# Performance work log

Hardware: AMD Instinct MI355X
Metric: run time of the kernel (lower is better)

The kernel has to match this reference:

```python
import jax, jax.numpy as jnp
import numpy as np

B, S, D = 4, 2048, 1024
E, H = 1024, 16
HD = E // H
TEMPERATURE = 1.0


def setup_inputs() -> dict:
    key = jax.random.key(0)
    ks = jax.random.split(key, 6)
    x = jax.random.normal(ks[0], (B, S, D), dtype=jnp.float32)
    src_key_padding_mask = jnp.zeros((B, S), dtype=bool)  # unused by module
    matrix_mask = jax.random.normal(ks[1], (B, S, S), dtype=jnp.float32)
    # Xavier-uniform linear weights (torch Linear stores [out, in])
    lim_qkv = float(np.sqrt(6.0 / (D + 3 * E)))
    qkv_w = jax.random.uniform(ks[2], (3 * E, D), dtype=jnp.float32, minval=-lim_qkv, maxval=lim_qkv)
    qkv_b = jnp.zeros((3 * E,), dtype=jnp.float32)
    lim_o = float(np.sqrt(6.0 / (E + E)))
    o_w = jax.random.uniform(ks[3], (E, E), dtype=jnp.float32, minval=-lim_o, maxval=lim_o)
    o_b = jnp.zeros((E,), dtype=jnp.float32)
    return {"x": x, "src_key_padding_mask": src_key_padding_mask, "matrix_mask": matrix_mask,
            "qkv_w": qkv_w, "qkv_b": qkv_b, "o_w": o_w, "o_b": o_b}


def reference(x, src_key_padding_mask, matrix_mask, qkv_w, qkv_b, o_w, o_b):
    b, s, _ = x.shape
    qkv = x @ qkv_w.T + qkv_b                      # [B,S,3E]
    qkv = qkv.reshape(b, s, H, 3 * HD).transpose(0, 2, 1, 3)  # [B,H,S,3*HD]
    q, k, v = jnp.split(qkv, 3, axis=-1)           # each [B,H,S,HD]
    scale = 1.0 / np.sqrt(HD)
    logits = jnp.einsum('bhqd,bhkd->bhqk', q, k) * scale + matrix_mask[:, None, :, :]
    attn = jax.nn.softmax(logits / TEMPERATURE, axis=-1)  # [B,H,S,S]
    # dropout=0.0, eval mode -> no-op
    values = jnp.einsum('bhqk,bhkd->bhqd', attn, v)       # [B,H,S,HD]
    values = values.transpose(0, 2, 1, 3).reshape(b, s, E)
    o = values @ o_w.T + o_b                       # [B,S,E]
    attention_mean = jnp.mean(attn, axis=1)        # [B,S,S]
    return (o, attention_mean)
```

## Files before the change

kernel.cpp:

```cpp
#include <hip/hip_runtime.h>

#define B_ 4
#define S_ 2048
#define D_ 1024
#define E_ 1024
#define H_ 16
#define HD_ 64
#define SCALE 0.125f
#define LOG2E 1.44269504f
#define C1_ (SCALE * LOG2E)

typedef __bf16 bf16;
typedef __bf16 bf16x8 __attribute__((ext_vector_type(8)));
typedef __bf16 bf16x4 __attribute__((ext_vector_type(4)));
typedef float f32x4 __attribute__((ext_vector_type(4)));
typedef _Float16 f16x8 __attribute__((ext_vector_type(8)));
typedef _Float16 f16x4 __attribute__((ext_vector_type(4)));

static __device__ __forceinline__ f32x4 mfma16(bf16x8 a, bf16x8 b, f32x4 c) {
  return __builtin_amdgcn_mfma_f32_16x16x32_bf16(a, b, c, 0, 0, 0);
}

typedef __attribute__((address_space(3))) void lvoid;
typedef const __attribute__((address_space(1))) void gvoid;
static __device__ __forceinline__ void gload16(const void* g, void* l) {
  __builtin_amdgcn_global_load_lds((gvoid*)g, (lvoid*)l, 16, 0, 0);
}

static __device__ __forceinline__ float exp2a(float x) {
  float r;
  asm("v_exp_f32 %0, %1" : "=v"(r) : "v"(x));
  return r;
}

static __device__ __forceinline__ int rsw(int row) {
  return (row & 3) | (((row >> 3) & 1) << 2);
}

__global__ void k_cvt(const float* __restrict__ in, bf16* __restrict__ out, int n4) {
  int i = blockIdx.x * 256 + threadIdx.x;
  if (i >= n4) return;
  float4 v = reinterpret_cast<const float4*>(in)[i];
  bf16x4 o = { (bf16)v.x, (bf16)v.y, (bf16)v.z, (bf16)v.w };
  reinterpret_cast<bf16x4*>(out)[i] = o;
}

__global__ void k_cvt16(const float* __restrict__ in, _Float16* __restrict__ out, int n4) {
  int i = blockIdx.x * 256 + threadIdx.x;
  if (i >= n4) return;
  float4 v = reinterpret_cast<const float4*>(in)[i];
  f16x4 o = { (_Float16)(v.x * LOG2E), (_Float16)(v.y * LOG2E),
              (_Float16)(v.z * LOG2E), (_Float16)(v.w * LOG2E) };
  reinterpret_cast<f16x4*>(out)[i] = o;
}

__global__ __launch_bounds__(256) void k_qkv(const bf16* __restrict__ xb,
                                             const bf16* __restrict__ wb,
                                             const float* __restrict__ qkvb,
                                             bf16* __restrict__ Qw,
                                             bf16* __restrict__ Kw,
                                             bf16* __restrict__ Vtw) {
  __shared__ __align__(16) bf16 lA[128 * 32];
  __shared__ __align__(16) bf16 lB[128 * 32];
  const int tid = threadIdx.x, lane = tid & 63, wv = tid >> 6;
  const int u = lane >> 4, c = lane & 15;
  const int wr = wv >> 1, wc = wv & 1;
  const int m0 = blockIdx.y * 128;
  const int n0 = blockIdx.x * 128;
  const int sr = tid >> 2, sk = (tid & 3) * 8;
  const bf16* gA = xb + (size_t)(m0 + sr) * D_ + sk;
  const bf16* gB = wb + (size_t)(n0 + sr) * D_ + sk;
  bf16* lpA = lA + wv * 512;
  bf16* lpB = lB + wv * 512;
  f32x4 acc[4][4] = {};
  for (int k0 = 0; k0 < D_; k0 += 32) {
    gload16(gA + k0, lpA);
    gload16(gA + 64 * D_ + k0, lpA + 2048);
    gload16(gB + k0, lpB);
    gload16(gB + 64 * D_ + k0, lpB + 2048);
    __syncthreads();
    bf16x8 af[4], bfr[4];
#pragma unroll
    for (int m = 0; m < 4; ++m)
      af[m] = *(const bf16x8*)(lA + (wr * 64 + m * 16 + c) * 32 + u * 8);
#pragma unroll
    for (int n = 0; n < 4; ++n)
      bfr[n] = *(const bf16x8*)(lB + (wc * 64 + n * 16 + c) * 32 + u * 8);
#pragma unroll
    for (int m = 0; m < 4; ++m)
#pragma unroll
      for (int n = 0; n < 4; ++n)
        acc[m][n] = mfma16(af[m], bfr[n], acc[m][n]);
    __syncthreads();
  }
#pragma unroll
  for (int n = 0; n < 4; ++n) {
    int nn = n0 + wc * 64 + n * 16 + c;
    float bias = qkvb[nn];
    int h = nn / 192;
    int rem = nn - h * 192;
#pragma unroll
    for (int m = 0; m < 4; ++m) {
#pragma unroll
      for (int r = 0; r < 4; ++r) {
        int q = m0 + wr * 64 + m * 16 + 4 * u + r;
        int bb = q >> 11, s = q & 2047;
        bf16 v = (bf16)(acc[m][n][r] + bias);
        if (rem < 64)       Qw[((bb * H_ + h) * S_ + s) * HD_ + rem] = v;
        else if (rem < 128) Kw[((bb * H_ + h) * S_ + s) * HD_ + (rem - 64)] = v;
        else                Vtw[((bb * H_ + h) * HD_ + (rem - 128)) * S_ + s] = v;
      }
    }
  }
}

#define PV_TILE2(HC, HN, BS, KT, PF)                                          \
  {                                                                           \
    f32x4 sA[4], sB[4];                                                       \
    _Pragma("unroll")                                                         \
    for (int f = 0; f < 4; ++f) {                                             \
      int rk = 32 * (f & 1) + 8 * (c >> 2) + 4 * (f >> 1) + (c & 3);          \
      int sw = rsw(rk);                                                       \
      bf16x8 k0 = *(const bf16x8*)&kl[BS][rk * 64 + ((u ^ sw) * 8)];          \
      bf16x8 k1 = *(const bf16x8*)&kl[BS][rk * 64 + (((4 + u) ^ sw) * 8)];    \
      f32x4 a = {};                                                           \
      a = mfma16(k0, aqA0, a);                                                \
      a = mfma16(k1, aqA1, a);                                                \
      sA[f] = a;                                                              \
      f32x4 bb2 = {};                                                         \
      bb2 = mfma16(k0, aqB0, bb2);                                            \
      bb2 = mfma16(k1, aqB1, bb2);                                            \
      sB[f] = bb2;                                                            \
    }                                                                         \
    if (PF) {                                                                 \
      const bf16* ksrc = Kb + (size_t)((KT) + 1) * 64 * HD_;                  \
      gload16(ksrc + ksw1, (bf16*)kl[(BS) ^ 1] + wv * 512);                   \
      gload16(ksrc + ksw2, (bf16*)kl[(BS) ^ 1] + 2048 + wv * 512);            \
      const bf16* vsrc = Vb + (size_t)((KT) + 1) * 64;                        \
      gload16(vsrc + vsw1, (bf16*)vl[(BS) ^ 1] + wv * 512);                   \
      gload16(vsrc + vsw2, (bf16*)vl[(BS) ^ 1] + 2048 + wv * 512);            \
      const _Float16* nA = bmrA + ((KT) + 1) * 64 + 8 * u;                    \
      const _Float16* nB = bmrB + ((KT) + 1) * 64 + 8 * u;                    \
      HN[0] = *(const f16x8*)(nA);                                            \
      HN[1] = *(const f16x8*)(nA + 32);                                       \
      HN[2] = *(const f16x8*)(nB);                                            \
      HN[3] = *(const f16x8*)(nB + 32);                                       \
    }                                                                         \
    float pA[16], pB[16];                                                     \
    _Pragma("unroll")                                                         \
    for (int f = 0; f < 4; ++f) {                                             \
      _Pragma("unroll")                                                       \
      for (int j = 0; j < 4; ++j) {                                           \
        float p = exp2a(sA[f][j] * C1_ + (float)HC[f & 1][4 * (f >> 1) + j]); \
        lsumA += p;                                                           \
        pA[f * 4 + j] = p;                                                    \
        float q2 = exp2a(sB[f][j] * C1_ +                                     \
                         (float)HC[2 + (f & 1)][4 * (f >> 1) + j]);           \
        lsumB += q2;                                                          \
        pB[f * 4 + j] = q2;                                                   \
      }                                                                       \
    }                                                                         \
    bf16x8 bpA0 = { (bf16)pA[0],  (bf16)pA[1],  (bf16)pA[2],  (bf16)pA[3],    \
                    (bf16)pA[8],  (bf16)pA[9],  (bf16)pA[10], (bf16)pA[11] }; \
    bf16x8 bpA1 = { (bf16)pA[4],  (bf16)pA[5],  (bf16)pA[6],  (bf16)pA[7],    \
                    (bf16)pA[12], (bf16)pA[13], (bf16)pA[14], (bf16)pA[15] }; \
    bf16x8 bpB0 = { (bf16)pB[0],  (bf16)pB[1],  (bf16)pB[2],  (bf16)pB[3],    \
                    (bf16)pB[8],  (bf16)pB[9],  (bf16)pB[10], (bf16)pB[11] }; \
    bf16x8 bpB1 = { (bf16)pB[4],  (bf16)pB[5],  (bf16)pB[6],  (bf16)pB[7],    \
                    (bf16)pB[12], (bf16)pB[13], (bf16)pB[14], (bf16)pB[15] }; \
    __builtin_amdgcn_s_setprio(1);                                            \
    _Pragma("unroll")                                                         \
    for (int g = 0; g < 4; ++g) {                                             \
      int rv = g * 16 + c;                                                    \
      int swv = rsw(rv);                                                      \
      bf16x8 v0 = *(const bf16x8*)&vl[BS][rv * 64 + ((u ^ swv) * 8)];         \
      bf16x8 v1 = *(const bf16x8*)&vl[BS][rv * 64 + (((4 + u) ^ swv) * 8)];   \
      accA[g] = mfma16(v0, bpA0, accA[g]);                                    \
      accA[g] = mfma16(v1, bpA1, accA[g]);                                    \
      accB[g] = mfma16(v0, bpB0, accB[g]);                                    \
      accB[g] = mfma16(v1, bpB1, accB[g]);                                    \
    }                                                                         \
    __builtin_amdgcn_s_setprio(0);                                            \
    __syncthreads();                                                          \
  }

__global__ __launch_bounds__(256) void k_pv(const bf16* __restrict__ Qw,
                                            const bf16* __restrict__ Kw,
                                            const bf16* __restrict__ Vtw,
                                            const _Float16* __restrict__ bmask,
                                            float* __restrict__ li_ws,
                                            bf16* __restrict__ valw) {
  __shared__ __align__(16) bf16 kl[2][64 * 64];
  __shared__ __align__(16) bf16 vl[2][64 * 64];
  const int tid = threadIdx.x, lane = tid & 63, wv = tid >> 6;
  const int u = lane >> 4, c = lane & 15;
  const int qt = blockIdx.x, h = blockIdx.y, b = blockIdx.z;
  const bf16* Qb = Qw + (size_t)(b * H_ + h) * S_ * HD_;
  const bf16* Kb = Kw + (size_t)(b * H_ + h) * S_ * HD_;
  const bf16* Vb = Vtw + (size_t)(b * H_ + h) * HD_ * S_;
  const int qrA = qt * 128 + wv * 32 + c;
  const int qrB = qrA + 16;
  bf16x8 aqA0 = *(const bf16x8*)(Qb + (size_t)qrA * HD_ + u * 8);
  bf16x8 aqA1 = *(const bf16x8*)(Qb + (size_t)qrA * HD_ + 32 + u * 8);
  bf16x8 aqB0 = *(const bf16x8*)(Qb + (size_t)qrB * HD_ + u * 8);
  bf16x8 aqB1 = *(const bf16x8*)(Qb + (size_t)qrB * HD_ + 32 + u * 8);
  const _Float16* bmrA = bmask + (size_t)b * S_ * S_ + (size_t)qrA * S_;
  const _Float16* bmrB = bmask + (size_t)b * S_ * S_ + (size_t)qrB * S_;
  const int r1 = tid >> 3, s1 = (tid & 7) ^ rsw(tid >> 3);
  const int g2i = tid + 256;
  const int r2 = g2i >> 3, s2 = (g2i & 7) ^ rsw(g2i >> 3);
  const int ksw1 = (r1 * 8 + s1) * 8, ksw2 = (r2 * 8 + s2) * 8;
  const int vsw1 = r1 * S_ + s1 * 8, vsw2 = r2 * S_ + s2 * 8;
  gload16(Kb + ksw1, (bf16*)kl[0] + wv * 512);
  gload16(Kb + ksw2, (bf16*)kl[0] + 2048 + wv * 512);
  gload16(Vb + vsw1, (bf16*)vl[0] + wv * 512);
  gload16(Vb + vsw2, (bf16*)vl[0] + 2048 + wv * 512);
  f16x8 hmA[4], hmB[4];
  hmA[0] = *(const f16x8*)(bmrA + 8 * u);
  hmA[1] = *(const f16x8*)(bmrA + 32 + 8 * u);
  hmA[2] = *(const f16x8*)(bmrB + 8 * u);
  hmA[3] = *(const f16x8*)(bmrB + 32 + 8 * u);
  f32x4 accA[4] = {}, accB[4] = {};
  float lsumA = 0.f, lsumB = 0.f;
  __syncthreads();
  for (int kt2 = 0; kt2 < 16; ++kt2) {
    PV_TILE2(hmA, hmB, 0, 2 * kt2, true);
    PV_TILE2(hmB, hmA, 1, 2 * kt2 + 1, (kt2 < 15));
  }
  lsumA += __shfl_xor(lsumA, 16, 64);
  lsumA += __shfl_xor(lsumA, 32, 64);
  lsumB += __shfl_xor(lsumB, 16, 64);
  lsumB += __shfl_xor(lsumB, 32, 64);
  float liA = 1.f / lsumA, liB = 1.f / lsumB;
  if (u == 0) {
    li_ws[(b * H_ + h) * S_ + qrA] = liA;
    li_ws[(b * H_ + h) * S_ + qrB] = liB;
  }
#pragma unroll
  for (int g = 0; g < 4; ++g) {
    bf16x4 pkA = { (bf16)(accA[g][0] * liA), (bf16)(accA[g][1] * liA),
                   (bf16)(accA[g][2] * liA), (bf16)(accA[g][3] * liA) };
    *(bf16x4*)(&valw[(size_t)(b * S_ + qrA) * E_ + h * HD_ + g * 16 + 4 * u]) = pkA;
    bf16x4 pkB = { (bf16)(accB[g][0] * liB), (bf16)(accB[g][1] * liB),
                   (bf16)(accB[g][2] * liB), (bf16)(accB[g][3] * liB) };
    *(bf16x4*)(&valw[(size_t)(b * S_ + qrB) * E_ + h * HD_ + g * 16 + 4 * u]) = pkB;
  }
}

#define MEAN_PHASE(QC0, QC1, QN0, QN1, BS, HH, PF)                             \
  {                                                                            \
    bf16x8 kf[8];                                                              \
    _Pragma("unroll")                                                          \
    for (int f = 0; f < 4; ++f) {                                              \
      int row = f * 16 + c;                                                    \
      int sw = row & 7;                                                        \
      kf[2 * f]     = *(const bf16x8*)&kl2[BS][row * 64 + ((u ^ sw) * 8)];     \
      kf[2 * f + 1] = *(const bf16x8*)&kl2[BS][row * 64 + (((4 + u) ^ sw) * 8)];\
    }                                                                          \
    if (PF) {                                                                  \
      const bf16* ksrc = Kw + (size_t)(bh0 + (HH) + 1) * S_ * HD_ +            \
                         (size_t)kt * 64 * HD_;                                \
      gload16(ksrc + sw1, (bf16*)kl2[(BS) ^ 1] + wv * 512);                    \
      gload16(ksrc + sw2, (bf16*)kl2[(BS) ^ 1] + 2048 + wv * 512);             \
      const bf16* Qn = Qw + (size_t)(bh0 + (HH) + 1) * S_ * HD_ +              \
                       (size_t)(qrow0 + c) * HD_ + u * 8;                      \
      QN0 = *(const bf16x8*)(Qn);                                              \
      QN1 = *(const bf16x8*)(Qn + 32);                                         \
    }                                                                          \
    float ll = li_l[(HH) * 64 + wv * 16 + c];                                  \
    f32x4 accf[4];                                                             \
    _Pragma("unroll")                                                          \
    for (int f = 0; f < 4; ++f) {                                              \
      f32x4 a = {};                                                            \
      a = mfma16(kf[2 * f], QC0, a);                                           \
      a = mfma16(kf[2 * f + 1], QC1, a);                                       \
      accf[f] = a;                                                             \
    }                                                                          \
    _Pragma("unroll")                                                          \
    for (int f = 0; f < 4; ++f) {                                              \
      _Pragma("unroll")                                                        \
      for (int j = 0; j < 4; ++j)                                              \
        macc[f][j] += exp2a(accf[f][j] * C1_ + mreg[f][j]) * ll;               \
    }                                                                          \
    __syncthreads();                                                           \
  }

__global__ __launch_bounds__(256) void k_mean(const bf16* __restrict__ Qw,
                                              const bf16* __restrict__ Kw,
                                              const _Float16* __restrict__ bmask,
                                              const float* __restrict__ li_ws,
                                              float* __restrict__ mean_out) {
  __shared__ float li_l[H_ * 64];
  __shared__ __align__(16) bf16 kl2[2][64 * 64];
  const int tid = threadIdx.x, lane = tid & 63, wv = tid >> 6;
  const int u = lane >> 4, c = lane & 15;
  const int qt = blockIdx.x, kt = blockIdx.y, b = blockIdx.z;
  const int bh0 = b * H_;
  for (int i = tid; i < H_ * 64; i += 256) {
    int hh = i >> 6, q = i & 63;
    li_l[i] = li_ws[(bh0 + hh) * S_ + qt * 64 + q];
  }
  const int qrow0 = qt * 64 + wv * 16;
  f32x4 mreg[4];
  {
    const _Float16* bmp = bmask + (size_t)b * S_ * S_ +
                          (size_t)(qrow0 + c) * S_ + (size_t)kt * 64 + 4 * u;
#pragma unroll
    for (int f = 0; f < 4; ++f) {
      f16x4 hv = *(const f16x4*)(bmp + f * 16);
      f32x4 mv = { (float)hv[0], (float)hv[1], (float)hv[2], (float)hv[3] };
      mreg[f] = mv;
    }
  }
  const int gg1 = wv * 64 + lane;
  const int gg2 = gg1 + 256;
  const int sw1 = (gg1 ^ ((gg1 >> 3) & 7)) * 8;
  const int sw2 = (gg2 ^ ((gg2 >> 3) & 7)) * 8;
  {
    const bf16* K0 = Kw + (size_t)bh0 * S_ * HD_ + (size_t)kt * 64 * HD_;
    gload16(K0 + sw1, (bf16*)kl2[0] + wv * 512);
    gload16(K0 + sw2, (bf16*)kl2[0] + 2048 + wv * 512);
  }
  bf16x8 qA0, qA1, qB0, qB1;
  {
    const bf16* Q0 = Qw + (size_t)bh0 * S_ * HD_ + (size_t)(qrow0 + c) * HD_ + u * 8;
    qA0 = *(const bf16x8*)Q0;
    qA1 = *(const bf16x8*)(Q0 + 32);
  }
  f32x4 macc[4] = {};
  __syncthreads();
  for (int h2 = 0; h2 < 8; ++h2) {
    MEAN_PHASE(qA0, qA1, qB0, qB1, 0, 2 * h2, true);
    MEAN_PHASE(qB0, qB1, qA0, qA1, 1, 2 * h2 + 1, (h2 < 7));
  }
#pragma unroll
  for (int f = 0; f < 4; ++f) {
    f32x4 mo = macc[f] * (1.f / 16.f);
    *(f32x4*)&mean_out[(size_t)b * S_ * S_ + (size_t)(qrow0 + c) * S_ +
                       (size_t)kt * 64 + f * 16 + 4 * u] = mo;
  }
}

__global__ __launch_bounds__(256) void k_oproj(const bf16* __restrict__ vb,
                                               const bf16* __restrict__ wo,
                                               const float* __restrict__ ob,
                                               float* __restrict__ out) {
  __shared__ __align__(16) bf16 lA[128 * 32];
  __shared__ __align__(16) bf16 lB[128 * 32];
  const int tid = threadIdx.x, lane = tid & 63, wv = tid >> 6;
  const int u = lane >> 4, c = lane & 15;
  const int wr = wv >> 1, wc = wv & 1;
  const int m0 = blockIdx.y * 128;
  const int n0 = blockIdx.x * 128;
  const int sr = tid >> 2, sk = (tid & 3) * 8;
  const bf16* gA = vb + (size_t)(m0 + sr) * E_ + sk;
  const bf16* gB = wo + (size_t)(n0 + sr) * E_ + sk;
  bf16* lpA = lA + wv * 512;
  bf16* lpB = lB + wv * 512;
  f32x4 acc[4][4] = {};
  for (int k0 = 0; k0 < E_; k0 += 32) {
    gload16(gA + k0, lpA);
    gload16(gA + 64 * E_ + k0, lpA + 2048);
    gload16(gB + k0, lpB);
    gload16(gB + 64 * E_ + k0, lpB + 2048);
    __syncthreads();
    bf16x8 af[4], bfr[4];
#pragma unroll
    for (int m = 0; m < 4; ++m)
      af[m] = *(const bf16x8*)(lA + (wr * 64 + m * 16 + c) * 32 + u * 8);
#pragma unroll
    for (int n = 0; n < 4; ++n)
      bfr[n] = *(const bf16x8*)(lB + (wc * 64 + n * 16 + c) * 32 + u * 8);
#pragma unroll
    for (int m = 0; m < 4; ++m)
#pragma unroll
      for (int n = 0; n < 4; ++n)
        acc[m][n] = mfma16(af[m], bfr[n], acc[m][n]);
    __syncthreads();
  }
#pragma unroll
  for (int n = 0; n < 4; ++n) {
    int nn = n0 + wc * 64 + n * 16 + c;
    float bias = ob[nn];
#pragma unroll
    for (int m = 0; m < 4; ++m) {
#pragma unroll
      for (int r = 0; r < 4; ++r) {
        int q = m0 + wr * 64 + m * 16 + 4 * u + r;
        out[(size_t)q * E_ + nn] = acc[m][n][r] + bias;
      }
    }
  }
}

extern "C" void kernel_launch(void* const* d_in, const int* in_sizes, int n_in,
                              void* d_out, int out_size, void* d_ws, size_t ws_size,
                              hipStream_t stream) {
  const float* x    = (const float*)d_in[0];
  const float* mmsk = (const float*)d_in[2];
  const float* qkvw = (const float*)d_in[3];
  const float* qkvb = (const float*)d_in[4];
  const float* ow   = (const float*)d_in[5];
  const float* ob   = (const float*)d_in[6];

  char* ws = (char*)d_ws;
  bf16* xb  = (bf16*)(ws);
  bf16* wb  = (bf16*)(ws + (16u << 20));
  bf16* owb = (bf16*)(ws + (22u << 20));
  bf16* Qw  = (bf16*)(ws + (24u << 20));
  bf16* Kw  = (bf16*)(ws + (40u << 20));
  bf16* Vtw = (bf16*)(ws + (56u << 20));
  float* li_ws = (float*)(ws + (16u << 20));
  bf16* values = xb;

  float* out_o    = (float*)d_out;
  float* out_mean = out_o + (size_t)B_ * S_ * E_;
  _Float16* bmask = (_Float16*)out_o;

  k_cvt<<<dim3(2097152 / 256), 256, 0, stream>>>(x, xb, 2097152);
  k_cvt<<<dim3(786432 / 256), 256, 0, stream>>>(qkvw, wb, 786432);
  k_cvt<<<dim3(262144 / 256), 256, 0, stream>>>(ow, owb, 262144);
  k_cvt16<<<dim3(4194304 / 256), 256, 0, stream>>>(mmsk, bmask, 4194304);
  k_qkv<<<dim3(24, 64), 256, 0, stream>>>(xb, wb, qkvb, Qw, Kw, Vtw);
  k_pv<<<dim3(16, 16, 4), 256, 0, stream>>>(Qw, Kw, Vtw, bmask, li_ws, values);
  k_mean<<<dim3(32, 32, 4), 256, 0, stream>>>(Qw, Kw, bmask, li_ws, out_mean);
  k_oproj<<<dim3(8, 64), 256, 0, stream>>>(values, owb, ob, out_o);
}
```

Baseline: 344.3 us.

## Issue K/V prefetch before QK compute and double query rows per mean block

In the attention-PV and mean kernels, the async global-to-LDS prefetch of the next K/V tile is now issued at the start of each tile, before the QK MFMAs. The full __syncthreads is replaced by a partial vmcnt wait plus s_barrier so the prefetch can stay in flight across iterations. The mean kernel now handles 128 query rows per block (two 64-row halves), so each K tile loaded into LDS serves twice as much work, and the grid halves. The mask is kept as f16 in registers and the exp is fused into the MFMA loop. This raises register pressure and relies on hand-counted vmcnt values being correct.

```diff
diff --git a/kernel.cpp b/kernel.cpp
--- a/kernel.cpp
+++ b/kernel.cpp
@@ -116,6 +116,15 @@
 
 #define PV_TILE2(HC, HN, BS, KT, PF)                                          \
   {                                                                           \
+    if (PF) {                                                                 \
+      const bf16* ksrc = Kb + (size_t)((KT) + 1) * 64 * HD_;                  \
+      gload16(ksrc + ksw1, (bf16*)kl[(BS) ^ 1] + wv * 512);                   \
+      gload16(ksrc + ksw2, (bf16*)kl[(BS) ^ 1] + 2048 + wv * 512);            \
+      const bf16* vsrc = Vb + (size_t)((KT) + 1) * 64;                        \
+      gload16(vsrc + vsw1, (bf16*)vl[(BS) ^ 1] + wv * 512);                   \
+      gload16(vsrc + vsw2, (bf16*)vl[(BS) ^ 1] + 2048 + wv * 512);            \
+      __builtin_amdgcn_sched_barrier(0);                                      \
+    }                                                                         \
     f32x4 sA[4], sB[4];                                                       \
     _Pragma("unroll")                                                         \
     for (int f = 0; f < 4; ++f) {                                             \
@@ -133,12 +142,6 @@
       sB[f] = bb2;                                                            \
     }                                                                         \
     if (PF) {                                                                 \
-      const bf16* ksrc = Kb + (size_t)((KT) + 1) * 64 * HD_;                  \
-      gload16(ksrc + ksw1, (bf16*)kl[(BS) ^ 1] + wv * 512);                   \
-      gload16(ksrc + ksw2, (bf16*)kl[(BS) ^ 1] + 2048 + wv * 512);            \
-      const bf16* vsrc = Vb + (size_t)((KT) + 1) * 64;                        \
-      gload16(vsrc + vsw1, (bf16*)vl[(BS) ^ 1] + wv * 512);                   \
-      gload16(vsrc + vsw2, (bf16*)vl[(BS) ^ 1] + 2048 + wv * 512);            \
       const _Float16* nA = bmrA + ((KT) + 1) * 64 + 8 * u;                    \
       const _Float16* nB = bmrB + ((KT) + 1) * 64 + 8 * u;                    \
       HN[0] = *(const f16x8*)(nA);                                            \
@@ -181,7 +184,8 @@
       accB[g] = mfma16(v1, bpB1, accB[g]);                                    \
     }                                                                         \
     __builtin_amdgcn_s_setprio(0);                                            \
-    __syncthreads();                                                          \
+    asm volatile("s_waitcnt vmcnt(4) lgkmcnt(0)" ::: "memory");               \
+    __builtin_amdgcn_s_barrier();                                             \
   }
 
 __global__ __launch_bounds__(256) void k_pv(const bf16* __restrict__ Qw,
@@ -247,8 +251,15 @@
   }
 }
 
-#define MEAN_PHASE(QC0, QC1, QN0, QN1, BS, HH, PF)                             \
+#define MEAN_PHASE(QC0, QC1, QC2, QC3, QN0, QN1, QN2, QN3, BS, HH, PF)         \
   {                                                                            \
+    if (PF) {                                                                  \
+      const bf16* ksrc = Kw + (size_t)(bh0 + (HH) + 1) * S_ * HD_ +            \
+                         (size_t)kt * 64 * HD_;                                \
+      gload16(ksrc + sw1, (bf16*)kl2[(BS) ^ 1] + wv * 512);                    \
+      gload16(ksrc + sw2, (bf16*)kl2[(BS) ^ 1] + 2048 + wv * 512);             \
+      __builtin_amdgcn_sched_barrier(0);                                       \
+    }                                                                          \
     bf16x8 kf[8];                                                              \
     _Pragma("unroll")                                                          \
     for (int f = 0; f < 4; ++f) {                                              \
@@ -258,31 +269,31 @@
       kf[2 * f + 1] = *(const bf16x8*)&kl2[BS][row * 64 + (((4 + u) ^ sw) * 8)];\
     }                                                                          \
     if (PF) {                                                                  \
-      const bf16* ksrc = Kw + (size_t)(bh0 + (HH) + 1) * S_ * HD_ +            \
-                         (size_t)kt * 64 * HD_;                                \
-      gload16(ksrc + sw1, (bf16*)kl2[(BS) ^ 1] + wv * 512);                    \
-      gload16(ksrc + sw2, (bf16*)kl2[(BS) ^ 1] + 2048 + wv * 512);             \
       const bf16* Qn = Qw + (size_t)(bh0 + (HH) + 1) * S_ * HD_ +              \
                        (size_t)(qrow0 + c) * HD_ + u * 8;                      \
       QN0 = *(const bf16x8*)(Qn);                                              \
       QN1 = *(const bf16x8*)(Qn + 32);                                         \
+      QN2 = *(const bf16x8*)(Qn + 64 * HD_);                                   \
+      QN3 = *(const bf16x8*)(Qn + 64 * HD_ + 32);                              \
     }                                                                          \
-    float ll = li_l[(HH) * 64 + wv * 16 + c];                                  \
-    f32x4 accf[4];                                                             \
+    float llA = li_l[(HH) * 128 + wv * 16 + c];                                \
+    float llB = li_l[(HH) * 128 + 64 + wv * 16 + c];                           \
     _Pragma("unroll")                                                          \
     for (int f = 0; f < 4; ++f) {                                              \
       f32x4 a = {};                                                            \
       a = mfma16(kf[2 * f], QC0, a);                                           \
       a = mfma16(kf[2 * f + 1], QC1, a);                                       \
-      accf[f] = a;                                                             \
+      f32x4 bb = {};                                                           \
+      bb = mfma16(kf[2 * f], QC2, bb);                                         \
+      bb = mfma16(kf[2 * f + 1], QC3, bb);                                     \
+      _Pragma("unroll")                                                        \
+      for (int j = 0; j < 4; ++j) {                                            \
+        maccA[f][j] += exp2a(a[j] * C1_ + (float)mhA[f][j]) * llA;             \
+        maccB[f][j] += exp2a(bb[j] * C1_ + (float)mhB[f][j]) * llB;            \
+      }                                                                        \
     }                                                                          \
-    _Pragma("unroll")                                                          \
-    for (int f = 0; f < 4; ++f) {                                              \
-      _Pragma("unroll")                                                        \
-      for (int j = 0; j < 4; ++j)                                              \
-        macc[f][j] += exp2a(accf[f][j] * C1_ + mreg[f][j]) * ll;               \
-    }                                                                          \
-    __syncthreads();                                                           \
+    asm volatile("s_waitcnt vmcnt(4) lgkmcnt(0)" ::: "memory");                \
+    __builtin_amdgcn_s_barrier();                                              \
   }
 
 __global__ __launch_bounds__(256) void k_mean(const bf16* __restrict__ Qw,
@@ -290,26 +301,26 @@
                                               const _Float16* __restrict__ bmask,
                                               const float* __restrict__ li_ws,
                                               float* __restrict__ mean_out) {
-  __shared__ float li_l[H_ * 64];
+  __shared__ float li_l[H_ * 128];
   __shared__ __align__(16) bf16 kl2[2][64 * 64];
   const int tid = threadIdx.x, lane = tid & 63, wv = tid >> 6;
   const int u = lane >> 4, c = lane & 15;
   const int qt = blockIdx.x, kt = blockIdx.y, b = blockIdx.z;
   const int bh0 = b * H_;
-  for (int i = tid; i < H_ * 64; i += 256) {
-    int hh = i >> 6, q = i & 63;
-    li_l[i] = li_ws[(bh0 + hh) * S_ + qt * 64 + q];
-  }
-  const int qrow0 = qt * 64 + wv * 16;
-  f32x4 mreg[4];
+  for (int i = tid; i < H_ * 128; i += 256) {
+    int hh = i >> 7, q = i & 127;
+    li_l[i] = li_ws[(bh0 + hh) * S_ + qt * 128 + q];
+  }
+  const int qrow0 = qt * 128 + wv * 16;
+  f16x4 mhA[4], mhB[4];
   {
-    const _Float16* bmp = bmask + (size_t)b * S_ * S_ +
-                          (size_t)(qrow0 + c) * S_ + (size_t)kt * 64 + 4 * u;
+    const _Float16* bmpA = bmask + (size_t)b * S_ * S_ +
+                           (size_t)(qrow0 + c) * S_ + (size_t)kt * 64 + 4 * u;
+    const _Float16* bmpB = bmpA + (size_t)64 * S_;
 #pragma unroll
     for (int f = 0; f < 4; ++f) {
-      f16x4 hv = *(const f16x4*)(bmp + f * 16);
-      f32x4 mv = { (float)hv[0], (float)hv[1], (float)hv[2], (float)hv[3] };
-      mreg[f] = mv;
+      mhA[f] = *(const f16x4*)(bmpA + f * 16);
+      mhB[f] = *(const f16x4*)(bmpB + f * 16);
     }
   }
   const int gg1 = wv * 64 + lane;
@@ -321,23 +332,28 @@
     gload16(K0 + sw1, (bf16*)kl2[0] + wv * 512);
     gload16(K0 + sw2, (bf16*)kl2[0] + 2048 + wv * 512);
   }
-  bf16x8 qA0, qA1, qB0, qB1;
+  bf16x8 qA0, qA1, qA2, qA3, qB0, qB1, qB2, qB3;
   {
     const bf16* Q0 = Qw + (size_t)bh0 * S_ * HD_ + (size_t)(qrow0 + c) * HD_ + u * 8;
     qA0 = *(const bf16x8*)Q0;
     qA1 = *(const bf16x8*)(Q0 + 32);
-  }
-  f32x4 macc[4] = {};
+    qA2 = *(const bf16x8*)(Q0 + 64 * HD_);
+    qA3 = *(const bf16x8*)(Q0 + 64 * HD_ + 32);
+  }
+  f32x4 maccA[4] = {}, maccB[4] = {};
   __syncthreads();
   for (int h2 = 0; h2 < 8; ++h2) {
-    MEAN_PHASE(qA0, qA1, qB0, qB1, 0, 2 * h2, true);
-    MEAN_PHASE(qB0, qB1, qA0, qA1, 1, 2 * h2 + 1, (h2 < 7));
+    MEAN_PHASE(qA0, qA1, qA2, qA3, qB0, qB1, qB2, qB3, 0, 2 * h2, true);
+    MEAN_PHASE(qB0, qB1, qB2, qB3, qA0, qA1, qA2, qA3, 1, 2 * h2 + 1, (h2 < 7));
   }
 #pragma unroll
   for (int f = 0; f < 4; ++f) {
-    f32x4 mo = macc[f] * (1.f / 16.f);
+    f32x4 moA = maccA[f] * (1.f / 16.f);
     *(f32x4*)&mean_out[(size_t)b * S_ * S_ + (size_t)(qrow0 + c) * S_ +
-                       (size_t)kt * 64 + f * 16 + 4 * u] = mo;
+                       (size_t)kt * 64 + f * 16 + 4 * u] = moA;
+    f32x4 moB = maccB[f] * (1.f / 16.f);
+    *(f32x4*)&mean_out[(size_t)b * S_ * S_ + (size_t)(qrow0 + 64 + c) * S_ +
+                       (size_t)kt * 64 + f * 16 + 4 * u] = moB;
   }
 }
 
@@ -423,6 +439,6 @@
   k_cvt16<<<dim3(4194304 / 256), 256, 0, stream>>>(mmsk, bmask, 4194304);
   k_qkv<<<dim3(24, 64), 256, 0, stream>>>(xb, wb, qkvb, Qw, Kw, Vtw);
   k_pv<<<dim3(16, 16, 4), 256, 0, stream>>>(Qw, Kw, Vtw, bmask, li_ws, values);
-  k_mean<<<dim3(32, 32, 4), 256, 0, stream>>>(Qw, Kw, bmask, li_ws, out_mean);
+  k_mean<<<dim3(16, 32, 4), 256, 0, stream>>>(Qw, Kw, bmask, li_ws, out_mean);
   k_oproj<<<dim3(8, 64), 256, 0, stream>>>(values, owb, ob, out_o);
 }
```

Result: no change. 347.2 us (+0.9%).
